# Performance work log

Hardware: AMD Instinct MI355X
Metric: run time of the kernel (lower is better)

The kernel has to match this reference:

```python
import jax, jax.numpy as jnp
import numpy as np
import math

DIM, NH, HD = 4096, 32, 128
B, S = 2, 2048
MAX_SEQ, INIT_SLICE = 4096, 2048  # init_slice = max_seq_len - max_prompt_size
NEG = -1e9


def setup_inputs() -> dict:
    key = jax.random.key(0)
    ks = jax.random.split(key, 6)
    x = jax.random.normal(ks[0], (B, S, DIM), dtype=jnp.float32)
    scale = 1.0 / math.sqrt(DIM)
    wq = jax.random.normal(ks[1], (DIM, DIM), dtype=jnp.float32) * scale
    wk = jax.random.normal(ks[2], (DIM, DIM), dtype=jnp.float32) * scale
    wv = jax.random.normal(ks[3], (DIM, DIM), dtype=jnp.float32) * scale
    wo = jax.random.normal(ks[4], (DIM, DIM), dtype=jnp.float32) * scale
    # RoPE frequencies, viewed as real pairs [S, HD//2, 2] = (cos, sin)
    inv_freq = 1.0 / (10000.0 ** (jnp.arange(0, HD, 2, dtype=jnp.float32) / HD))
    ang = jnp.arange(S, dtype=jnp.float32)[:, None] * inv_freq[None, :]  # [S, HD//2]
    freqs_cis_real = jnp.stack([jnp.cos(ang), jnp.sin(ang)], axis=-1)
    # causal additive mask [1,1,S,S]
    mask = jnp.where(jnp.triu(jnp.ones((S, S), dtype=bool), k=1), NEG, 0.0)[None, None].astype(jnp.float32)
    cache_k = jnp.zeros((B, MAX_SEQ, NH, HD), dtype=jnp.float32)
    cache_v = jnp.zeros((B, MAX_SEQ, NH, HD), dtype=jnp.float32)
    return {"x": x, "freqs_cis_real": freqs_cis_real, "mask": mask,
            "wq": wq, "wk": wk, "wv": wv, "wo": wo,
            "cache_k": cache_k, "cache_v": cache_v, "slice_size": 2048}


def _apply_rotary(xq, xk, freqs_cis_real):
    # xq, xk: [b, s, h, d]; pairs along last dim are (real, imag)
    b, s, h, d = xq.shape
    fr = freqs_cis_real[None, :, None, :, 0]  # [1, s, 1, d//2]
    fi = freqs_cis_real[None, :, None, :, 1]

    def rot(t):
        t = t.reshape(b, s, h, d // 2, 2)
        tr, ti = t[..., 0], t[..., 1]
        out = jnp.stack([tr * fr - ti * fi, tr * fi + ti * fr], axis=-1)
        return out.reshape(b, s, h, d)

    return rot(xq), rot(xk)


def reference(x, freqs_cis_real, mask, wq, wk, wv, wo, cache_k, cache_v, slice_size):
    bsz, seqlen, _ = x.shape
    xq = (x @ wq.T).reshape(bsz, seqlen, NH, HD)
    xk = (x @ wk.T).reshape(bsz, seqlen, NH, HD)
    xv = (x @ wv.T).reshape(bsz, seqlen, NH, HD)
    xq, xk = _apply_rotary(xq, xk, freqs_cis_real)
    # prompt-phase (seqlen > 1) cache update: cat(cache[:, :init_slice], new)
    cache_k_new = jnp.concatenate([cache_k[:bsz, :INIT_SLICE], xk], axis=1)
    cache_v_new = jnp.concatenate([cache_v[:bsz, :INIT_SLICE], xv], axis=1)
    keys = cache_k_new[:, -slice_size:]    # [b, k, h, d]
    values = cache_v_new[:, -slice_size:]
    scores = jnp.einsum('bqhd,bkhd->bhqk', xq, keys) / math.sqrt(HD)
    scores = scores + mask
    probs = jax.nn.softmax(scores.astype(jnp.float32), axis=-1).astype(xq.dtype)
    out = jnp.einsum('bhqk,bkhd->bqhd', probs, values).reshape(bsz, seqlen, -1)
    return out @ wo.T
```

## Files before the change

### kernel.cpp

```cpp
#include <hip/hip_runtime.h>
#include <hip/hip_bf16.h>
#include <stdint.h>

#define SEQ   2048
#define NHEAD 32
#define HDIM  128
#define DMODEL 4096
#define MTOT  4096
#define RSCALE 0.08838834764831845f

typedef __hip_bfloat16 bf16_t;
typedef __attribute__((ext_vector_type(8))) short short8v;
typedef __attribute__((ext_vector_type(4))) short short4v;
typedef __attribute__((ext_vector_type(4))) float f32x4;

typedef __attribute__((address_space(3))) void lds_void;
typedef __attribute__((address_space(1))) void gbl_void;
#define TO_LDS(p) ((lds_void*)(uint32_t)(uintptr_t)(p))
#define TO_GBL(p) ((gbl_void*)(uintptr_t)(p))
#define ASYNC_CP16(g, l) __builtin_amdgcn_global_load_lds(TO_GBL(g), TO_LDS(l), 16, 0, 0)

__device__ __forceinline__ float bf2f(short u) {
  union { uint32_t i; float f; } x; x.i = ((uint32_t)(uint16_t)u) << 16; return x.f;
}

__global__ __launch_bounds__(256) void cast4_f32_to_bf16(const float* __restrict__ s0,
                                                         const float* __restrict__ s1,
                                                         const float* __restrict__ s2,
                                                         const float* __restrict__ s3,
                                                         bf16_t* __restrict__ out) {
  const int w = blockIdx.y;
  const float* in = (w == 0) ? s0 : ((w == 1) ? s1 : ((w == 2) ? s2 : s3));
  bf16_t* o = out + (size_t)w * 16777216u;
  size_t i = (size_t)blockIdx.x * 256 + threadIdx.x;
  const f32x4* p = (const f32x4*)in + i * 2;
  f32x4 a = p[0], b = p[1];
  __align__(16) bf16_t tmp[8];
#pragma unroll
  for (int j = 0; j < 4; ++j) tmp[j]     = __float2bfloat16(a[j]);
#pragma unroll
  for (int j = 0; j < 4; ++j) tmp[4 + j] = __float2bfloat16(b[j]);
  *(short8v*)(o + i * 8) = *(const short8v*)tmp;
}

__global__ __launch_bounds__(256) void cast_f32_to_bf16(const float* __restrict__ in,
                                                        bf16_t* __restrict__ out) {
  size_t i = (size_t)blockIdx.x * 256 + threadIdx.x;
  const f32x4* p = (const f32x4*)in + i * 2;
  f32x4 a = p[0], b = p[1];
  __align__(16) bf16_t tmp[8];
#pragma unroll
  for (int j = 0; j < 4; ++j) tmp[j]     = __float2bfloat16(a[j]);
#pragma unroll
  for (int j = 0; j < 4; ++j) tmp[4 + j] = __float2bfloat16(b[j]);
  *(short8v*)(out + i * 8) = *(const short8v*)tmp;
}

#define VMW_(N) asm volatile("s_waitcnt vmcnt(" #N ")" ::: "memory")
#define VMW(N) VMW_(N)
#define SB0 __builtin_amdgcn_sched_barrier(0)

#define STAGE_A(mh_, X)                                                        \
  { const int tr_ = tid >> 3, c_ = tid & 7;                                    \
    _Pragma("unroll")                                                          \
    for (int i_ = 0; i_ < 2; ++i_) {                                           \
      const int row_ = (mh_) * 64 + i_ * 128 + tr_;                            \
      const int cg_ = c_ ^ (row_ & 7);                                         \
      ASYNC_CP16(gA0 + (size_t)row_ * 4096 + (size_t)(X) * 64 + cg_ * 8,       \
                 ldsc + (((X) & 1) << 16) + row_ * 128 + c_ * 16); } }

#define STAGE_B(nh_, X)                                                        \
  { const int tr_ = tid >> 3, c_ = tid & 7;                                    \
    _Pragma("unroll")                                                          \
    for (int i_ = 0; i_ < 2; ++i_) {                                           \
      const int row_ = i_ * 128 + (tr_ >> 5) * 64 + (nh_) * 32 + (tr_ & 31);   \
      const int cg_ = c_ ^ (row_ & 7);                                         \
      ASYNC_CP16(gB0 + (size_t)row_ * 4096 + (size_t)(X) * 64 + cg_ * 8,       \
                 ldsc + (((X) & 1) << 16) + 32768 + row_ * 128 + c_ * 16); } }

#define TILE4(T, DOSTG, VA, VB, VC)                                            \
  {                                                                            \
    const int sb = ((T) & 1) << 16;                                            \
    const int Xn = (T) + 1;                                                    \
    short8v a0[4][2], a1[4][2], b0[2][2], b1[2][2];                            \
                                                 \
    VMW(VA);                                                                   \
    __builtin_amdgcn_s_barrier();                                              \
    SB0;                                                                       \
    _Pragma("unroll") for (int m = 0; m < 4; ++m)                              \
      _Pragma("unroll") for (int kk = 0; kk < 2; ++kk)                         \
        a0[m][kk] = *(const short8v*)(ldsc + sb + aRow + m * 2048 + (kk ? cx1 : cx0)); \
    _Pragma("unroll") for (int n = 0; n < 2; ++n)                              \
      _Pragma("unroll") for (int kk = 0; kk < 2; ++kk)                         \
        b0[n][kk] = *(const short8v*)(ldsc + sb + bRow + n * 2048 + (kk ? cx1 : cx0)); \
    if (DOSTG) STAGE_A(0, Xn);                                                 \
    asm volatile("s_waitcnt lgkmcnt(0)" ::: "memory");                         \
    SB0;                                                                       \
    __builtin_amdgcn_s_setprio(1);                                             \
    _Pragma("unroll") for (int m = 0; m < 4; ++m)                              \
      _Pragma("unroll") for (int n = 0; n < 2; ++n)                            \
        _Pragma("unroll") for (int kk = 0; kk < 2; ++kk)                       \
          acc[m][n] = __builtin_amdgcn_mfma_f32_16x16x32_bf16(a0[m][kk], b0[n][kk], acc[m][n], 0, 0, 0); \
    __builtin_amdgcn_s_setprio(0);                                             \
                                                 \
    VMW(VB);                                                                   \
    __builtin_amdgcn_s_barrier();                                              \
    SB0;                                                                       \
    _Pragma("unroll") for (int n = 0; n < 2; ++n)                              \
      _Pragma("unroll") for (int kk = 0; kk < 2; ++kk)                         \
        b1[n][kk] = *(const short8v*)(ldsc + sb + bRow + 4096 + n * 2048 + (kk ? cx1 : cx0)); \
    if (DOSTG) STAGE_B(0, Xn);                                                 \
    asm volatile("s_waitcnt lgkmcnt(0)" ::: "memory");                         \
    SB0;                                                                       \
    __builtin_amdgcn_s_setprio(1);                                             \
    _Pragma("unroll") for (int m = 0; m < 4; ++m)                              \
      _Pragma("unroll") for (int n = 0; n < 2; ++n)                            \
        _Pragma("unroll") for (int kk = 0; kk < 2; ++kk)                       \
          acc[m][2 + n] = __builtin_amdgcn_mfma_f32_16x16x32_bf16(a0[m][kk], b1[n][kk], acc[m][2 + n], 0, 0, 0); \
    __builtin_amdgcn_s_setprio(0);                                             \
                                                 \
    VMW(VC);                                                                   \
    __builtin_amdgcn_s_barrier();                                              \
    SB0;                                                                       \
    _Pragma("unroll") for (int m = 0; m < 4; ++m)                              \
      _Pragma("unroll") for (int kk = 0; kk < 2; ++kk)                         \
        a1[m][kk] = *(const short8v*)(ldsc + sb + aRow + 8192 + m * 2048 + (kk ? cx1 : cx0)); \
    if (DOSTG) STAGE_B(1, Xn);                                                 \
    asm volatile("s_waitcnt lgkmcnt(0)" ::: "memory");                         \
    SB0;                                                                       \
    __builtin_amdgcn_s_setprio(1);                                             \
    _Pragma("unroll") for (int m = 0; m < 4; ++m)                              \
      _Pragma("unroll") for (int n = 0; n < 2; ++n)                            \
        _Pragma("unroll") for (int kk = 0; kk < 2; ++kk)                       \
          acc[4 + m][2 + n] = __builtin_amdgcn_mfma_f32_16x16x32_bf16(a1[m][kk], b1[n][kk], acc[4 + m][2 + n], 0, 0, 0); \
    __builtin_amdgcn_s_setprio(0);                                             \
                                     \
    if (DOSTG) STAGE_A(1, Xn);                                                 \
    __builtin_amdgcn_s_setprio(1);                                             \
    _Pragma("unroll") for (int m = 0; m < 4; ++m)                              \
      _Pragma("unroll") for (int n = 0; n < 2; ++n)                            \
        _Pragma("unroll") for (int kk = 0; kk < 2; ++kk)                       \
          acc[4 + m][n] = __builtin_amdgcn_mfma_f32_16x16x32_bf16(a1[m][kk], b0[n][kk], acc[4 + m][n], 0, 0, 0); \
    __builtin_amdgcn_s_setprio(0);                                             \
  }

template <int MODE>
__global__ __launch_bounds__(512, 2) void gemm_nt(const bf16_t* __restrict__ A,
                                                  const bf16_t* __restrict__ B0,
                                                  const bf16_t* __restrict__ B1,
                                                  const bf16_t* __restrict__ B2,
                                                  void* __restrict__ out0,
                                                  bf16_t* __restrict__ out1,
                                                  bf16_t* __restrict__ out2,
                                                  const float* __restrict__ freqs) {
  __shared__ __align__(16) char ldsbuf[131072];
  char* ldsc = ldsbuf;
  const int z = blockIdx.z;
  const bf16_t* __restrict__ Bm = (z == 0) ? B0 : (z == 1 ? B1 : B2);
  const int tid = threadIdx.x;
  const int wave = tid >> 6, lane = tid & 63;
  const int bid = blockIdx.x;
  const int xcd = bid & 7, idx = bid >> 3;
  const int bm = xcd * 2 + (idx >> 4);
  const int bn = idx & 15;
  const int wr = wave >> 2, wc = wave & 3;
  const int r = lane & 15, g = lane >> 4;

  f32x4 acc[8][4] = {};

  const bf16_t* gA0 = A  + (size_t)bm * 256 * 4096;
  const bf16_t* gB0 = Bm + (size_t)bn * 256 * 4096;

  const int swz = r & 7;
  const int cx0 = (g ^ swz) << 4;
  const int cx1 = ((4 + g) ^ swz) << 4;
  const int aRow = (wr * 128 + r) * 128;
  const int bRow = 32768 + (wc * 64 + r) * 128;

  STAGE_A(0, 0);
  STAGE_B(0, 0);
  STAGE_B(1, 0);
  STAGE_A(1, 0);

  for (int T = 0; T < 63; ++T) TILE4(T, 1, 4, 4, 4);
  TILE4(63, 0, 4, 2, 0);

  const int row0 = bm * 256 + wr * 128 + g * 4;
  const int col0 = bn * 256 + wc * 64;

  if (MODE == 0) {
    float* C = (float*)out0;
#pragma unroll
    for (int m = 0; m < 8; ++m)
#pragma unroll
      for (int n = 0; n < 4; ++n)
#pragma unroll
        for (int j = 0; j < 4; ++j)
          C[(size_t)(row0 + m * 16 + j) * 4096 + col0 + n * 16 + r] = acc[m][n][j];
  } else if (z == 2) {
    bf16_t* VT = out2;
#pragma unroll
    for (int m = 0; m < 8; ++m) {
      const int row = row0 + m * 16;
      const int b = row >> 11, s = row & 2047;
#pragma unroll
      for (int n = 0; n < 4; ++n) {
        const int col = col0 + n * 16 + r;
        const int h = col >> 7, d = col & 127;
        __align__(8) bf16_t tp[4];
#pragma unroll
        for (int j = 0; j < 4; ++j) tp[j] = __float2bfloat16(acc[m][n][j]);
        *(short4v*)&VT[((size_t)(b * 32 + h) * 128 + d) * 2048 + s] = *(const short4v*)tp;
      }
    }
  } else {
    bf16_t* dst = (z == 0) ? (bf16_t*)out0 : out1;
    const float scl = (z == 0) ? RSCALE : 1.0f;
    const float sgn = (r & 1) ? 1.0f : -1.0f;
#pragma unroll
    for (int m = 0; m < 8; ++m)
#pragma unroll
      for (int j = 0; j < 4; ++j) {
        const int row = row0 + m * 16 + j;
        const int b = row >> 11, s = row & 2047;
#pragma unroll
        for (int n = 0; n < 4; ++n) {
          const int col = col0 + n * 16 + r;
          const int h = col >> 7, d = col & 127;
          const float self = acc[m][n][j];
          const float part = __shfl_xor(self, 1, 64);
          const float* fp = freqs + (size_t)s * 128 + (d >> 1) * 2;
          const float frv = fp[0] * scl;
          const float fiv = fp[1] * scl * sgn;
          dst[((size_t)(b * 32 + h) * 2048 + s) * 128 + d] =
              __float2bfloat16(self * frv + part * fiv);
        }
      }
  }
}

#define PSTR 72
__global__ __launch_bounds__(512) void attn_kernel(const bf16_t* __restrict__ qrot,
                                                   const bf16_t* __restrict__ krot,
                                                   const bf16_t* __restrict__ vt,
                                                   bf16_t* __restrict__ att) {
  __shared__ bf16_t Kls[3][64 * 128];
  __shared__ bf16_t Vls[3][128 * 64];
  __shared__ bf16_t Pls[8][16 * PSTR];

  const int lid  = blockIdx.x;
  const int xcd  = lid & 7;
  const int kk_  = lid >> 3;
  const int bh   = xcd + 8 * ((kk_ >> 4) & 7);
  const int qidx = 15 - (kk_ & 15);
  const int warp = threadIdx.x >> 6;
  const int lane = threadIdx.x & 63;
  const int r = lane & 15, g = lane >> 4;

  const bf16_t* __restrict__ Q  = qrot + (size_t)bh * 2048 * 128;
  const bf16_t* __restrict__ Kp = krot + (size_t)bh * 2048 * 128;
  const bf16_t* __restrict__ Vt = vt   + (size_t)bh * 128 * 2048;
  bf16_t* __restrict__ Pw = &Pls[warp][0];

  const int qB = qidx * 128 + warp * 16;
  const int ntiles = 2 * qidx + 2;

  short8v qf[4];
#pragma unroll
  for (int kk = 0; kk < 4; ++kk)
    qf[kk] = *(const short8v*)&Q[(size_t)(qB + r) * 128 + kk * 32 + g * 8];

  float l = 0.f;
  f32x4 o[8];
#pragma unroll
  for (int n2 = 0; n2 < 8; ++n2) o[n2] = f32x4{0.f, 0.f, 0.f, 0.f};

  const int rA = lane >> 4, cA = lane & 15;
  const int rB = lane >> 3, cB = lane & 7;
  const int swz = (r & 7) << 4;

  auto STG = [&](int kb_, int buf) {
#pragma unroll
    for (int i = 0; i < 2; ++i) {
      const int krow = warp * 8 + i * 4 + rA;
      const int kcol = 8 * (cA ^ (krow & 7));
      ASYNC_CP16(Kp + (size_t)(kb_ + krow) * 128 + kcol,
                 (char*)&Kls[buf][0] + (size_t)(krow * 128 + cA * 8) * 2);
    }
#pragma unroll
    for (int i = 0; i < 2; ++i) {
      const int vrow = warp * 16 + i * 8 + rB;
      const int vcol = 8 * (cB ^ rB);
      ASYNC_CP16(Vt + (size_t)vrow * 2048 + kb_ + vcol,
                 (char*)&Vls[buf][0] + (size_t)(vrow * 64 + cB * 8) * 2);
    }
  };

  STG(0, 0);
  int cur = 0;
  for (int t = 0; t < ntiles; ++t) {
    const int kb = t * 64;
    const int nxt = (cur == 2) ? 0 : cur + 1;
    if (t + 1 < ntiles) {
      STG(kb + 64, nxt);
      VMW(4);
    } else {
      VMW(0);
    }
    __builtin_amdgcn_s_barrier();
    SB0;

    if (kb <= qB + 15) {
      const char* Kc = (const char*)&Kls[cur][0];
      const char* Vc = (const char*)&Vls[cur][0];
      f32x4 sacc[4];
#pragma unroll
      for (int n = 0; n < 4; ++n) sacc[n] = f32x4{0.f, 0.f, 0.f, 0.f};
#pragma unroll
      for (int n = 0; n < 4; ++n)
#pragma unroll
        for (int kk = 0; kk < 4; ++kk) {
          short8v kf = *(const short8v*)(Kc + (n * 16 + r) * 256 + ((kk * 64 + g * 16) ^ swz));
          sacc[n] = __builtin_amdgcn_mfma_f32_16x16x32_bf16(kf, qf[kk], sacc[n], 0, 0, 0);
        }

      float p[16];
#pragma unroll
      for (int n = 0; n < 4; ++n)
#pragma unroll
        for (int j = 0; j < 4; ++j)
          p[n * 4 + j] = __expf(sacc[n][j]);

      if (kb + 63 > qB) {
        const int qa = qB + r;
#pragma unroll
        for (int n = 0; n < 4; ++n)
#pragma unroll
          for (int j = 0; j < 4; ++j)
            if (kb + n * 16 + g * 4 + j > qa) p[n * 4 + j] = 0.f;
      }

      {
        float ts[8];
#pragma unroll
        for (int i = 0; i < 8; ++i) ts[i] = p[i] + p[i + 8];
#pragma unroll
        for (int i = 0; i < 4; ++i) ts[i] += ts[i + 4];
        float rs = (ts[0] + ts[1]) + (ts[2] + ts[3]);
        rs += __shfl_xor(rs, 16, 64);
        rs += __shfl_xor(rs, 32, 64);
        l += rs;
      }

#pragma unroll
      for (int n = 0; n < 4; ++n) {
        __align__(8) bf16_t tp[4];
#pragma unroll
        for (int j = 0; j < 4; ++j) tp[j] = __float2bfloat16(p[n * 4 + j]);
        *(short4v*)&Pw[r * PSTR + n * 16 + g * 4] = *(const short4v*)tp;
      }

#pragma unroll
      for (int kk2 = 0; kk2 < 2; ++kk2) {
        short8v pf = *(const short8v*)&Pw[r * PSTR + kk2 * 32 + g * 8];
#pragma unroll
        for (int n2 = 0; n2 < 8; ++n2) {
          short8v vf = *(const short8v*)(Vc + (n2 * 16 + r) * 128 + ((kk2 * 64 + g * 16) ^ swz));
          o[n2] = __builtin_amdgcn_mfma_f32_16x16x32_bf16(pf, vf, o[n2], 0, 0, 0);
        }
      }
    }
    cur = nxt;
  }

  float lq[4];
#pragma unroll
  for (int j = 0; j < 4; ++j) lq[j] = 1.0f / __shfl(l, g * 4 + j, 64);
  const int b = bh >> 5, h = bh & 31;
#pragma unroll
  for (int n2 = 0; n2 < 8; ++n2)
#pragma unroll
    for (int j = 0; j < 4; ++j)
      att[((size_t)(b * 2048 + qB + g * 4 + j)) * 4096 + h * 128 + n2 * 16 + r] =
          __float2bfloat16(o[n2][j] * lq[j]);
}

extern "C" void kernel_launch(void* const* d_in, const int* in_sizes, int n_in,
                              void* d_out, int out_size, void* d_ws, size_t ws_size,
                              hipStream_t stream) {
  (void)in_sizes; (void)n_in; (void)out_size; (void)ws_size;
  const float* x  = (const float*)d_in[0];
  const float* fr = (const float*)d_in[1];
  const float* wq = (const float*)d_in[3];
  const float* wk = (const float*)d_in[4];
  const float* wv = (const float*)d_in[5];
  const float* wo = (const float*)d_in[6];

  char* ws = (char*)d_ws;
  const size_t MB32 = 33554432;
  bf16_t* xb   = (bf16_t*)(ws + 0 * MB32);
  bf16_t* wqb  = (bf16_t*)(ws + 1 * MB32);
  bf16_t* wkb  = (bf16_t*)(ws + 2 * MB32);
  bf16_t* wvb  = (bf16_t*)(ws + 3 * MB32);
  bf16_t* qrot = (bf16_t*)(ws + 4 * MB32);
  bf16_t* krot = (bf16_t*)(ws + 5 * MB32);
  bf16_t* vtp  = (bf16_t*)(ws + 6 * MB32);

  cast4_f32_to_bf16<<<dim3(8192, 4), 256, 0, stream>>>(x, wq, wk, wv, xb);

  gemm_nt<1><<<dim3(256, 1, 3), 512, 0, stream>>>(xb, wqb, wkb, wvb,
                                                  (void*)qrot, krot, vtp, fr);

  bf16_t* wob  = wqb;
  bf16_t* attb = xb;
  cast_f32_to_bf16<<<8192, 256, 0, stream>>>(wo, wob);

  attn_kernel<<<1024, 512, 0, stream>>>(qrot, krot, vtp, attb);

  gemm_nt<0><<<dim3(256, 1, 1), 512, 0, stream>>>(attb, wob, wob, wob,
                                                  d_out, nullptr, nullptr, nullptr);
}
```

Before: 654.9 us.

## Move Q RoPE into attention, switch to double-buffered K/V with swizzled P LDS

Q rotary embedding and softmax scaling move out of the GEMM epilogue and into the attention kernel's Q-fragment load, so the GEMM writes plain Q. The attention K/V staging drops from a triple buffer with a partial vmcnt wait to a double buffer with a full wait and barrier at the end of each tile. The padded P scratch is replaced by an XOR-swizzled 64-wide layout. Together these cut LDS use per block, which may raise occupancy, but the full wait each tile gives less overlap of loads with compute.

```diff
diff --git a/kernel.cpp b/kernel.cpp
--- a/kernel.cpp
+++ b/kernel.cpp
@@ -13,6 +13,7 @@
 typedef __attribute__((ext_vector_type(8))) short short8v;
 typedef __attribute__((ext_vector_type(4))) short short4v;
 typedef __attribute__((ext_vector_type(4))) float f32x4;
+typedef __attribute__((ext_vector_type(2))) float f32x2;
 
 typedef __attribute__((address_space(3))) void lds_void;
 typedef __attribute__((address_space(1))) void gbl_void;
@@ -213,9 +214,23 @@
         *(short4v*)&VT[((size_t)(b * 32 + h) * 128 + d) * 2048 + s] = *(const short4v*)tp;
       }
     }
+  } else if (z == 0) {
+    bf16_t* dst = (bf16_t*)out0;
+#pragma unroll
+    for (int m = 0; m < 8; ++m)
+#pragma unroll
+      for (int j = 0; j < 4; ++j) {
+        const int row = row0 + m * 16 + j;
+        const int b = row >> 11, s = row & 2047;
+#pragma unroll
+        for (int n = 0; n < 4; ++n) {
+          const int col = col0 + n * 16 + r;
+          const int h = col >> 7, d = col & 127;
+          dst[((size_t)(b * 32 + h) * 2048 + s) * 128 + d] = __float2bfloat16(acc[m][n][j]);
+        }
+      }
   } else {
-    bf16_t* dst = (z == 0) ? (bf16_t*)out0 : out1;
-    const float scl = (z == 0) ? RSCALE : 1.0f;
+    bf16_t* dst = out1;
     const float sgn = (r & 1) ? 1.0f : -1.0f;
 #pragma unroll
     for (int m = 0; m < 8; ++m)
@@ -230,8 +245,8 @@
           const float self = acc[m][n][j];
           const float part = __shfl_xor(self, 1, 64);
           const float* fp = freqs + (size_t)s * 128 + (d >> 1) * 2;
-          const float frv = fp[0] * scl;
-          const float fiv = fp[1] * scl * sgn;
+          const float frv = fp[0];
+          const float fiv = fp[1] * sgn;
           dst[((size_t)(b * 32 + h) * 2048 + s) * 128 + d] =
               __float2bfloat16(self * frv + part * fiv);
         }
@@ -239,14 +254,14 @@
   }
 }
 
-#define PSTR 72
 __global__ __launch_bounds__(512) void attn_kernel(const bf16_t* __restrict__ qrot,
                                                    const bf16_t* __restrict__ krot,
                                                    const bf16_t* __restrict__ vt,
+                                                   const float* __restrict__ freqs,
                                                    bf16_t* __restrict__ att) {
-  __shared__ bf16_t Kls[3][64 * 128];
-  __shared__ bf16_t Vls[3][128 * 64];
-  __shared__ bf16_t Pls[8][16 * PSTR];
+  __shared__ bf16_t Kls[2][64 * 128];
+  __shared__ bf16_t Vls[2][128 * 64];
+  __shared__ bf16_t Pls[8][16 * 64];
 
   const int lid  = blockIdx.x;
   const int xcd  = lid & 7;
@@ -260,15 +275,31 @@
   const bf16_t* __restrict__ Q  = qrot + (size_t)bh * 2048 * 128;
   const bf16_t* __restrict__ Kp = krot + (size_t)bh * 2048 * 128;
   const bf16_t* __restrict__ Vt = vt   + (size_t)bh * 128 * 2048;
-  bf16_t* __restrict__ Pw = &Pls[warp][0];
+  char* __restrict__ Pb = (char*)&Pls[warp][0];
 
   const int qB = qidx * 128 + warp * 16;
   const int ntiles = 2 * qidx + 2;
+  const int psw = (r & 7) << 4;
 
   short8v qf[4];
-#pragma unroll
-  for (int kk = 0; kk < 4; ++kk)
-    qf[kk] = *(const short8v*)&Q[(size_t)(qB + r) * 128 + kk * 32 + g * 8];
+  {
+    const int s = qB + r;
+    const float* fbase = freqs + (size_t)s * 128;
+#pragma unroll
+    for (int kk = 0; kk < 4; ++kk) {
+      short8v qraw = *(const short8v*)&Q[(size_t)s * 128 + kk * 32 + g * 8];
+      __align__(16) bf16_t qt[8];
+#pragma unroll
+      for (int i = 0; i < 4; ++i) {
+        const int p = kk * 16 + g * 4 + i;
+        f32x2 cs = *(const f32x2*)(fbase + p * 2);
+        const float a = bf2f(qraw[2 * i]), b = bf2f(qraw[2 * i + 1]);
+        qt[2 * i]     = __float2bfloat16((a * cs[0] - b * cs[1]) * RSCALE);
+        qt[2 * i + 1] = __float2bfloat16((a * cs[1] + b * cs[0]) * RSCALE);
+      }
+      qf[kk] = *(const short8v*)qt;
+    }
+  }
 
   float l = 0.f;
   f32x4 o[8];
@@ -297,18 +328,12 @@
   };
 
   STG(0, 0);
+  VMW(0);
+  __builtin_amdgcn_s_barrier();
   int cur = 0;
   for (int t = 0; t < ntiles; ++t) {
     const int kb = t * 64;
-    const int nxt = (cur == 2) ? 0 : cur + 1;
-    if (t + 1 < ntiles) {
-      STG(kb + 64, nxt);
-      VMW(4);
-    } else {
-      VMW(0);
-    }
-    __builtin_amdgcn_s_barrier();
-    SB0;
+    if (t + 1 < ntiles) STG(kb + 64, cur ^ 1);
 
     if (kb <= qB + 15) {
       const char* Kc = (const char*)&Kls[cur][0];
@@ -357,12 +382,12 @@
         __align__(8) bf16_t tp[4];
 #pragma unroll
         for (int j = 0; j < 4; ++j) tp[j] = __float2bfloat16(p[n * 4 + j]);
-        *(short4v*)&Pw[r * PSTR + n * 16 + g * 4] = *(const short4v*)tp;
+        *(short4v*)(Pb + r * 128 + ((n * 32 + g * 8) ^ psw)) = *(const short4v*)tp;
       }
 
 #pragma unroll
       for (int kk2 = 0; kk2 < 2; ++kk2) {
-        short8v pf = *(const short8v*)&Pw[r * PSTR + kk2 * 32 + g * 8];
+        short8v pf = *(const short8v*)(Pb + r * 128 + ((kk2 * 64 + g * 16) ^ psw));
 #pragma unroll
         for (int n2 = 0; n2 < 8; ++n2) {
           short8v vf = *(const short8v*)(Vc + (n2 * 16 + r) * 128 + ((kk2 * 64 + g * 16) ^ swz));
@@ -370,7 +395,12 @@
         }
       }
     }
-    cur = nxt;
+
+    if (t + 1 < ntiles) {
+      VMW(0);
+      __builtin_amdgcn_s_barrier();
+    }
+    cur ^= 1;
   }
 
   float lq[4];
@@ -415,7 +445,7 @@
   bf16_t* attb = xb;
   cast_f32_to_bf16<<<8192, 256, 0, stream>>>(wo, wob);
 
-  attn_kernel<<<1024, 512, 0, stream>>>(qrot, krot, vtp, attb);
+  attn_kernel<<<1024, 512, 0, stream>>>(qrot, krot, vtp, fr, attb);
 
   gemm_nt<0><<<dim3(256, 1, 1), 512, 0, stream>>>(attb, wob, wob, wob,
                                                   d_out, nullptr, nullptr, nullptr);
```

Measured after the change: 647.0 us. No clear change (-1.2%).
